# Optimization experiments

Measured on AMD Instinct MI355X. Metric: run time of the kernel, lower is better.

Reference implementation:

```python
import jax, jax.numpy as jnp
import numpy as np

N_NODES = 100000
N_EDGES = 3200000
IN_DIM, HID_DIM, OUT_DIM = 768, 50, 2


def gcn_conv(x, W, b, row, col, deg_isqrt, n_nodes):
    # PyG GCNConv: h = x @ W, then symmetric-normalized scatter-add (self-loops
    # already included in row/col), then + bias.
    h = x @ W                                    # [N, out]
    norm = deg_isqrt[row] * deg_isqrt[col]       # [E+N]
    msgs = h[row] * norm[:, None]                # gather + scale
    out = jax.ops.segment_sum(msgs, col, num_segments=n_nodes)
    return out + b


def _augment(edge_index, n_nodes):
    # add self-loops and compute D^{-1/2} with self-loops
    loops = jnp.arange(n_nodes, dtype=edge_index.dtype)
    row = jnp.concatenate([edge_index[0], loops])
    col = jnp.concatenate([edge_index[1], loops])
    deg = jax.ops.segment_sum(jnp.ones_like(col, dtype=jnp.float32), col,
                              num_segments=n_nodes)
    deg_isqrt = jnp.where(deg > 0, jax.lax.rsqrt(deg), 0.0)
    return row, col, deg_isqrt


def setup_inputs() -> dict:
    key = jax.random.key(0)
    k1, k2, k3, k4 = jax.random.split(key, 4)
    x = jax.random.normal(k1, (N_NODES, IN_DIM), dtype=jnp.float32)
    edge_index = jax.random.randint(k2, (2, N_EDGES), 0, N_NODES, dtype=jnp.int64)
    W1 = jax.random.normal(k3, (IN_DIM, HID_DIM), dtype=jnp.float32) / np.sqrt(IN_DIM)
    b1 = jnp.zeros((HID_DIM,), dtype=jnp.float32)
    W2 = jax.random.normal(k4, (HID_DIM, OUT_DIM), dtype=jnp.float32) / np.sqrt(HID_DIM)
    b2 = jnp.zeros((OUT_DIM,), dtype=jnp.float32)
    return {"x": x, "edge_index": edge_index, "W1": W1, "b1": b1, "W2": W2, "b2": b2}


def reference(x, edge_index, W1, b1, W2, b2):
    n = x.shape[0]
    row, col, deg_isqrt = _augment(edge_index, n)
    h = gcn_conv(x, W1, b1, row, col, deg_isqrt, n)   # GCNConv(768 -> 50)
    h = jax.nn.relu(h)                                 # ReLU
    h = gcn_conv(h, W2, b2, row, col, deg_isqrt, n)   # GCNConv(50 -> 2)
    return jax.nn.sigmoid(h)                           # Sigmoid output layer
```

## Files before the change

### kernel.cpp

```cpp
#include <hip/hip_runtime.h>


#define N_NODES 100000
#define N_EDGES 3200000
#define IN_DIM  768
#define HID     50
#define HIDP    52
#define SCAN_BLK 1024
#define NSCAN_BLKS 98
#define NPAD (NSCAN_BLKS * SCAN_BLK)

using s8v = __attribute__((ext_vector_type(8))) short;
using f4v = __attribute__((ext_vector_type(4))) float;

__device__ __forceinline__ short f2bf(float f) {
  union { float f; unsigned u; } v; v.f = f;
  unsigned r = (v.u + 0x7fffu + ((v.u >> 16) & 1u)) >> 16;
  return (short)r;
}
__device__ __forceinline__ float bf2f(unsigned short u) {
  union { unsigned u; float f; } v; v.u = ((unsigned)u) << 16;
  return v.f;
}


__global__ void k_init(int* __restrict__ cnt) {
  int g = blockIdx.x * 256 + threadIdx.x;
  if (g < NPAD) cnt[g] = 0;
}

__global__ void k_count(const int* __restrict__ edges, int* __restrict__ cnt) {
  int e = blockIdx.x * 256 + threadIdx.x;
  if (e < N_EDGES) atomicAdd(&cnt[edges[N_EDGES + e]], 1);
}

__global__ void k_scanA(const int* __restrict__ cnt, int* __restrict__ offs,
                        int* __restrict__ bsum) {
  __shared__ int s[SCAN_BLK];
  int t = threadIdx.x;
  int g = blockIdx.x * SCAN_BLK + t;
  int v = (g < N_NODES) ? cnt[g] : 0;
  s[t] = v;
  __syncthreads();
  for (int off = 1; off < SCAN_BLK; off <<= 1) {
    int add = (t >= off) ? s[t - off] : 0;
    __syncthreads();
    s[t] += add;
    __syncthreads();
  }
  offs[g] = s[t] - v;
  if (t == SCAN_BLK - 1) bsum[blockIdx.x] = s[t];
}

__global__ void k_scanB(int* __restrict__ bsum) {
  if (threadIdx.x == 0 && blockIdx.x == 0) {
    int acc = 0;
    for (int i = 0; i < NSCAN_BLKS; ++i) { int v = bsum[i]; bsum[i] = acc; acc += v; }
  }
}

__global__ void k_scanC(int* __restrict__ cnt, int* __restrict__ offs,
                        const int* __restrict__ bsum, float* __restrict__ dis) {
  int g = blockIdx.x * 256 + threadIdx.x;
  if (g < NPAD) {
    offs[g] += bsum[g >> 10];
    if (g < N_NODES) {
      dis[g] = rsqrtf((float)cnt[g] + 1.0f);
      cnt[g] = 0;
    }
  }
}

__global__ void k_fill(const int* __restrict__ edges, int* __restrict__ cnt,
                       const int* __restrict__ offs, int* __restrict__ eidx) {
  int e = blockIdx.x * 256 + threadIdx.x;
  if (e < N_EDGES) {
    int r = edges[e];
    int c = edges[N_EDGES + e];
    int p = atomicAdd(&cnt[c], 1);
    eidx[offs[c] + p] = r;
  }
}


__global__ __launch_bounds__(256) void k_gemm1(const float* __restrict__ x,
                                               const float* __restrict__ W1,
                                               unsigned short* __restrict__ h1) {
  __shared__ short BT[64][72];
  int t = threadIdx.x;
  int wave = t >> 6, lane = t & 63;
  int col = lane & 15, quad = lane >> 4;
  int rb = blockIdx.x * 64 + wave * 16;
  int arow = rb + col;
  if (arow > N_NODES - 1) arow = N_NODES - 1;
  const float* xrow = x + (size_t)arow * IN_DIM + quad * 8;

  f4v acc[4] = {f4v{0.f,0.f,0.f,0.f}, f4v{0.f,0.f,0.f,0.f},
                f4v{0.f,0.f,0.f,0.f}, f4v{0.f,0.f,0.f,0.f}};

  for (int chunk = 0; chunk < IN_DIM / 64; ++chunk) {
    int k0 = chunk * 64;
    __syncthreads();
    for (int e = t; e < 64 * 64; e += 256) {
      int k = e >> 6, n = e & 63;
      float v = (n < HID) ? W1[(k0 + k) * HID + n] : 0.f;
      BT[n][k] = f2bf(v);
    }
    __syncthreads();
    for (int kk = 0; kk < 64; kk += 32) {
      float4 va = *(const float4*)(xrow + k0 + kk);
      float4 vb = *(const float4*)(xrow + k0 + kk + 4);
      s8v a;
      a[0] = f2bf(va.x); a[1] = f2bf(va.y); a[2] = f2bf(va.z); a[3] = f2bf(va.w);
      a[4] = f2bf(vb.x); a[5] = f2bf(vb.y); a[6] = f2bf(vb.z); a[7] = f2bf(vb.w);
      s8v b0 = *(const s8v*)&BT[ 0 + col][kk + quad * 8];
      s8v b1 = *(const s8v*)&BT[16 + col][kk + quad * 8];
      s8v b2 = *(const s8v*)&BT[32 + col][kk + quad * 8];
      s8v b3 = *(const s8v*)&BT[48 + col][kk + quad * 8];
      acc[0] = __builtin_amdgcn_mfma_f32_16x16x32_bf16(a, b0, acc[0], 0, 0, 0);
      acc[1] = __builtin_amdgcn_mfma_f32_16x16x32_bf16(a, b1, acc[1], 0, 0, 0);
      acc[2] = __builtin_amdgcn_mfma_f32_16x16x32_bf16(a, b2, acc[2], 0, 0, 0);
      acc[3] = __builtin_amdgcn_mfma_f32_16x16x32_bf16(a, b3, acc[3], 0, 0, 0);
    }
  }
  for (int nt = 0; nt < 4; ++nt) {
    int c = nt * 16 + col;
    if (c < HIDP) {
      for (int r = 0; r < 4; ++r) {
        int node = rb + quad * 4 + r;
        if (node < N_NODES)
          h1[(size_t)node * HIDP + c] = (unsigned short)f2bf(acc[nt][r]);
      }
    }
  }
}


__global__ __launch_bounds__(256) void k_agg1(
    const unsigned short* __restrict__ h1, const int* __restrict__ eidx,
    const int* __restrict__ offs, const float* __restrict__ dis,
    const float* __restrict__ b1, const float* __restrict__ W2,
    float* __restrict__ h2) {
  __shared__ float W2s[2][HIDP];
  __shared__ float b1s[HIDP];
  int t = threadIdx.x;
  if (t < HIDP) {
    b1s[t] = (t < HID) ? b1[t] : 0.f;
    W2s[0][t] = (t < HID) ? W2[t * 2 + 0] : 0.f;
    W2s[1][t] = (t < HID) ? W2[t * 2 + 1] : 0.f;
  }
  __syncthreads();
  int g = t >> 4, L = t & 15;
  int n = blockIdx.x * 16 + g;
  if (n >= N_NODES) return;
  int start = offs[n];
  int end = (n == N_NODES - 1) ? N_EDGES : offs[n + 1];
  int base = L * 4;
  bool act = base < HIDP;
  float a0 = 0.f, a1 = 0.f, a2 = 0.f, a3 = 0.f;
  for (int i = start; i < end; ++i) {
    int idx = eidx[i];
    float d = dis[idx];
    if (act) {
      ushort4 u = *(const ushort4*)(h1 + (size_t)idx * HIDP + base);
      a0 += bf2f(u.x) * d; a1 += bf2f(u.y) * d;
      a2 += bf2f(u.z) * d; a3 += bf2f(u.w) * d;
    }
  }
  float p0 = 0.f, p1 = 0.f;
  if (act) {
    float dn = dis[n];
    ushort4 u = *(const ushort4*)(h1 + (size_t)n * HIDP + base);
    a0 = a0 * dn + bf2f(u.x) * dn * dn + b1s[base + 0];
    a1 = a1 * dn + bf2f(u.y) * dn * dn + b1s[base + 1];
    a2 = a2 * dn + bf2f(u.z) * dn * dn + b1s[base + 2];
    a3 = a3 * dn + bf2f(u.w) * dn * dn + b1s[base + 3];
    a0 = fmaxf(a0, 0.f); a1 = fmaxf(a1, 0.f);
    a2 = fmaxf(a2, 0.f); a3 = fmaxf(a3, 0.f);
    p0 = a0 * W2s[0][base] + a1 * W2s[0][base + 1] +
         a2 * W2s[0][base + 2] + a3 * W2s[0][base + 3];
    p1 = a0 * W2s[1][base] + a1 * W2s[1][base + 1] +
         a2 * W2s[1][base + 2] + a3 * W2s[1][base + 3];
  }
  for (int m = 8; m; m >>= 1) {
    p0 += __shfl_xor(p0, m, 16);
    p1 += __shfl_xor(p1, m, 16);
  }
  if (L == 0) {
    h2[(size_t)n * 2 + 0] = p0;
    h2[(size_t)n * 2 + 1] = p1;
  }
}


__global__ __launch_bounds__(256) void k_agg2(
    const float* __restrict__ h2, const int* __restrict__ eidx,
    const int* __restrict__ offs, const float* __restrict__ dis,
    const float* __restrict__ b2, float* __restrict__ out) {
  int t = threadIdx.x;
  int g = t >> 4, L = t & 15;
  int n = blockIdx.x * 16 + g;
  if (n >= N_NODES) return;
  int start = offs[n];
  int end = (n == N_NODES - 1) ? N_EDGES : offs[n + 1];
  float a0 = 0.f, a1 = 0.f;
  for (int i = start + L; i < end; i += 16) {
    int idx = eidx[i];
    float d = dis[idx];
    float2 v = *(const float2*)(h2 + (size_t)idx * 2);
    a0 += v.x * d; a1 += v.y * d;
  }
  for (int m = 8; m; m >>= 1) {
    a0 += __shfl_xor(a0, m, 16);
    a1 += __shfl_xor(a1, m, 16);
  }
  if (L == 0) {
    float dn = dis[n];
    float2 v = *(const float2*)(h2 + (size_t)n * 2);
    float r0 = a0 * dn + v.x * dn * dn + b2[0];
    float r1 = a1 * dn + v.y * dn * dn + b2[1];
    out[(size_t)n * 2 + 0] = 1.f / (1.f + __expf(-r0));
    out[(size_t)n * 2 + 1] = 1.f / (1.f + __expf(-r1));
  }
}


static inline size_t aln(size_t v) { return (v + 255) & ~(size_t)255; }

extern "C" void kernel_launch(void* const* d_in, const int* in_sizes, int n_in,
                              void* d_out, int out_size, void* d_ws, size_t ws_size,
                              hipStream_t stream) {
  const float* x     = (const float*)d_in[0];
  const int*   edges = (const int*)d_in[1];
  const float* W1    = (const float*)d_in[2];
  const float* b1    = (const float*)d_in[3];
  const float* W2    = (const float*)d_in[4];
  const float* b2    = (const float*)d_in[5];
  float* out = (float*)d_out;

  char* p = (char*)d_ws;
  int* cnt  = (int*)p;            p += aln((size_t)NPAD * 4);
  int* offs = (int*)p;            p += aln((size_t)NPAD * 4);
  int* bsum = (int*)p;            p += aln((size_t)NSCAN_BLKS * 4);
  float* dis = (float*)p;         p += aln((size_t)N_NODES * 4);
  int* eidx = (int*)p;            p += aln((size_t)N_EDGES * 4);
  unsigned short* h1 = (unsigned short*)p; p += aln((size_t)N_NODES * HIDP * 2);
  float* h2 = (float*)p;          p += aln((size_t)N_NODES * 2 * 4);

  int gN   = (NPAD + 255) / 256;
  int gE   = (N_EDGES + 255) / 256;
  int gMM  = (N_NODES + 63) / 64;
  int gAgg = (N_NODES + 15) / 16;

  k_init <<<gN, 256, 0, stream>>>(cnt);
  k_count<<<gE, 256, 0, stream>>>(edges, cnt);
  k_scanA<<<NSCAN_BLKS, SCAN_BLK, 0, stream>>>(cnt, offs, bsum);
  k_scanB<<<1, 64, 0, stream>>>(bsum);
  k_scanC<<<gN, 256, 0, stream>>>(cnt, offs, bsum, dis);
  k_fill <<<gE, 256, 0, stream>>>(edges, cnt, offs, eidx);
  k_gemm1<<<gMM, 256, 0, stream>>>(x, W1, h1);
  k_agg1 <<<gAgg, 256, 0, stream>>>(h1, eidx, offs, dis, b1, W2, h2);
  k_agg2 <<<gAgg, 256, 0, stream>>>(h2, eidx, offs, dis, b2, out);
}
```

Before: 938.9 us.

## Prescale features by source degree, prepack W1 fragments, widen aggregation to waves

h1 is now stored pre-multiplied by deg^-1/2 of the source node in the GEMM epilogue, so the aggregation loops no longer gather dis[idx] per edge. The same is done for the second-layer features. W1 is converted once into bf16 MFMA fragment order by a new prep kernel, which removes the per-block LDS transpose and its barriers from the GEMM. Each aggregation now uses one wave per node: agg1 splits edges four ways with a software-prefetched gather, and agg2 uses 64 lanes. The block-sum scan is parallelised and the counter init kernel becomes a memset. Per-node wave mapping may waste lanes on low-degree nodes, and the extra bf16 rounding after scaling slightly changes numerics.

Measured after the change: 839.2 us. 1.12x faster.

```diff
diff --git a/kernel.cpp b/kernel.cpp
--- a/kernel.cpp
+++ b/kernel.cpp
@@ -9,6 +9,7 @@
 #define SCAN_BLK 1024
 #define NSCAN_BLKS 98
 #define NPAD (NSCAN_BLKS * SCAN_BLK)
+#define NKSTEP (IN_DIM / 32)
 
 using s8v = __attribute__((ext_vector_type(8))) short;
 using f4v = __attribute__((ext_vector_type(4))) float;
@@ -23,11 +24,6 @@
   return v.f;
 }
 
-
-__global__ void k_init(int* __restrict__ cnt) {
-  int g = blockIdx.x * 256 + threadIdx.x;
-  if (g < NPAD) cnt[g] = 0;
-}
 
 __global__ void k_count(const int* __restrict__ edges, int* __restrict__ cnt) {
   int e = blockIdx.x * 256 + threadIdx.x;
@@ -53,10 +49,18 @@
 }
 
 __global__ void k_scanB(int* __restrict__ bsum) {
-  if (threadIdx.x == 0 && blockIdx.x == 0) {
-    int acc = 0;
-    for (int i = 0; i < NSCAN_BLKS; ++i) { int v = bsum[i]; bsum[i] = acc; acc += v; }
-  }
+  __shared__ int s[128];
+  int t = threadIdx.x;
+  int v = (t < NSCAN_BLKS) ? bsum[t] : 0;
+  s[t] = v;
+  __syncthreads();
+  for (int off = 1; off < 128; off <<= 1) {
+    int add = (t >= off) ? s[t - off] : 0;
+    __syncthreads();
+    s[t] += add;
+    __syncthreads();
+  }
+  if (t < NSCAN_BLKS) bsum[t] = s[t] - v;
 }
 
 __global__ void k_scanC(int* __restrict__ cnt, int* __restrict__ offs,
@@ -83,10 +87,25 @@
 }
 
 
+__global__ void k_wprep(const float* __restrict__ W1, short* __restrict__ Bfrag) {
+  int g = blockIdx.x * 256 + threadIdx.x;
+  int s = g >> 8, r = g & 255;
+  int nt = r >> 6, l = r & 63;
+  int col = l & 15, quad = l >> 4;
+  int n = nt * 16 + col;
+  int kb = s * 32 + quad * 8;
+  s8v o;
+#pragma unroll
+  for (int j = 0; j < 8; ++j)
+    o[j] = (n < HID) ? f2bf(W1[(size_t)(kb + j) * HID + n]) : (short)0;
+  *(s8v*)(Bfrag + (size_t)g * 8) = o;
+}
+
+
 __global__ __launch_bounds__(256) void k_gemm1(const float* __restrict__ x,
-                                               const float* __restrict__ W1,
+                                               const short* __restrict__ Bfrag,
+                                               const float* __restrict__ dis,
                                                unsigned short* __restrict__ h1) {
-  __shared__ short BT[64][72];
   int t = threadIdx.x;
   int wave = t >> 6, lane = t & 63;
   int col = lane & 15, quad = lane >> 4;
@@ -94,42 +113,42 @@
   int arow = rb + col;
   if (arow > N_NODES - 1) arow = N_NODES - 1;
   const float* xrow = x + (size_t)arow * IN_DIM + quad * 8;
+  const short* bbase = Bfrag + (size_t)lane * 8;
 
   f4v acc[4] = {f4v{0.f,0.f,0.f,0.f}, f4v{0.f,0.f,0.f,0.f},
                 f4v{0.f,0.f,0.f,0.f}, f4v{0.f,0.f,0.f,0.f}};
 
-  for (int chunk = 0; chunk < IN_DIM / 64; ++chunk) {
-    int k0 = chunk * 64;
-    __syncthreads();
-    for (int e = t; e < 64 * 64; e += 256) {
-      int k = e >> 6, n = e & 63;
-      float v = (n < HID) ? W1[(k0 + k) * HID + n] : 0.f;
-      BT[n][k] = f2bf(v);
-    }
-    __syncthreads();
-    for (int kk = 0; kk < 64; kk += 32) {
-      float4 va = *(const float4*)(xrow + k0 + kk);
-      float4 vb = *(const float4*)(xrow + k0 + kk + 4);
-      s8v a;
-      a[0] = f2bf(va.x); a[1] = f2bf(va.y); a[2] = f2bf(va.z); a[3] = f2bf(va.w);
-      a[4] = f2bf(vb.x); a[5] = f2bf(vb.y); a[6] = f2bf(vb.z); a[7] = f2bf(vb.w);
-      s8v b0 = *(const s8v*)&BT[ 0 + col][kk + quad * 8];
-      s8v b1 = *(const s8v*)&BT[16 + col][kk + quad * 8];
-      s8v b2 = *(const s8v*)&BT[32 + col][kk + quad * 8];
-      s8v b3 = *(const s8v*)&BT[48 + col][kk + quad * 8];
-      acc[0] = __builtin_amdgcn_mfma_f32_16x16x32_bf16(a, b0, acc[0], 0, 0, 0);
-      acc[1] = __builtin_amdgcn_mfma_f32_16x16x32_bf16(a, b1, acc[1], 0, 0, 0);
-      acc[2] = __builtin_amdgcn_mfma_f32_16x16x32_bf16(a, b2, acc[2], 0, 0, 0);
-      acc[3] = __builtin_amdgcn_mfma_f32_16x16x32_bf16(a, b3, acc[3], 0, 0, 0);
-    }
-  }
+#pragma unroll
+  for (int s = 0; s < NKSTEP; ++s) {
+    float4 va = *(const float4*)(xrow + s * 32);
+    float4 vb = *(const float4*)(xrow + s * 32 + 4);
+    s8v b0 = *(const s8v*)(bbase + (size_t)(s * 4 + 0) * 512);
+    s8v b1 = *(const s8v*)(bbase + (size_t)(s * 4 + 1) * 512);
+    s8v b2 = *(const s8v*)(bbase + (size_t)(s * 4 + 2) * 512);
+    s8v b3 = *(const s8v*)(bbase + (size_t)(s * 4 + 3) * 512);
+    s8v a;
+    a[0] = f2bf(va.x); a[1] = f2bf(va.y); a[2] = f2bf(va.z); a[3] = f2bf(va.w);
+    a[4] = f2bf(vb.x); a[5] = f2bf(vb.y); a[6] = f2bf(vb.z); a[7] = f2bf(vb.w);
+    acc[0] = __builtin_amdgcn_mfma_f32_16x16x32_bf16(a, b0, acc[0], 0, 0, 0);
+    acc[1] = __builtin_amdgcn_mfma_f32_16x16x32_bf16(a, b1, acc[1], 0, 0, 0);
+    acc[2] = __builtin_amdgcn_mfma_f32_16x16x32_bf16(a, b2, acc[2], 0, 0, 0);
+    acc[3] = __builtin_amdgcn_mfma_f32_16x16x32_bf16(a, b3, acc[3], 0, 0, 0);
+  }
+
+  int node0 = rb + quad * 4;
+  float dd[4];
+#pragma unroll
+  for (int r = 0; r < 4; ++r)
+    dd[r] = (node0 + r < N_NODES) ? dis[node0 + r] : 0.f;
+#pragma unroll
   for (int nt = 0; nt < 4; ++nt) {
     int c = nt * 16 + col;
     if (c < HIDP) {
+#pragma unroll
       for (int r = 0; r < 4; ++r) {
-        int node = rb + quad * 4 + r;
+        int node = node0 + r;
         if (node < N_NODES)
-          h1[(size_t)node * HIDP + c] = (unsigned short)f2bf(acc[nt][r]);
+          h1[(size_t)node * HIDP + c] = (unsigned short)f2bf(acc[nt][r] * dd[r]);
       }
     }
   }
@@ -140,85 +159,97 @@
     const unsigned short* __restrict__ h1, const int* __restrict__ eidx,
     const int* __restrict__ offs, const float* __restrict__ dis,
     const float* __restrict__ b1, const float* __restrict__ W2,
-    float* __restrict__ h2) {
-  __shared__ float W2s[2][HIDP];
-  __shared__ float b1s[HIDP];
-  int t = threadIdx.x;
-  if (t < HIDP) {
+    float* __restrict__ h2s) {
+  __shared__ float W2s[2][64];
+  __shared__ float b1s[64];
+  int t = threadIdx.x;
+  if (t < 64) {
     b1s[t] = (t < HID) ? b1[t] : 0.f;
     W2s[0][t] = (t < HID) ? W2[t * 2 + 0] : 0.f;
     W2s[1][t] = (t < HID) ? W2[t * 2 + 1] : 0.f;
   }
   __syncthreads();
-  int g = t >> 4, L = t & 15;
-  int n = blockIdx.x * 16 + g;
+  int wave = t >> 6, lane = t & 63;
+  int n = blockIdx.x * 4 + wave;
+  if (n >= N_NODES) return;
+  int way = lane >> 4, L = lane & 15;
+  int base = L * 4;
+  bool actC = base < HIDP;
+  int baseS = actC ? base : 0;
+  int start = offs[n];
+  int end = (n == N_NODES - 1) ? N_EDGES : offs[n + 1];
+
+  float a0 = 0.f, a1 = 0.f, a2 = 0.f, a3 = 0.f;
+  int i  = start + way;
+  int idx  = (i  < end) ? eidx[i]  : n;
+  ushort4 u = *(const ushort4*)(h1 + (size_t)idx * HIDP + baseS);
+  int i2 = i + 4;
+  int idx2 = (i2 < end) ? eidx[i2] : n;
+  while (i < end) {
+    ushort4 u2 = *(const ushort4*)(h1 + (size_t)idx2 * HIDP + baseS);
+    int i3 = i2 + 4;
+    int idx3 = (i3 < end) ? eidx[i3] : n;
+    a0 += bf2f(u.x); a1 += bf2f(u.y); a2 += bf2f(u.z); a3 += bf2f(u.w);
+    u = u2; idx2 = idx3; i = i2; i2 = i3;
+  }
+
+  a0 += __shfl_xor(a0, 16); a0 += __shfl_xor(a0, 32);
+  a1 += __shfl_xor(a1, 16); a1 += __shfl_xor(a1, 32);
+  a2 += __shfl_xor(a2, 16); a2 += __shfl_xor(a2, 32);
+  a3 += __shfl_xor(a3, 16); a3 += __shfl_xor(a3, 32);
+
+  float p0 = 0.f, p1 = 0.f;
+  if (actC && way == 0) {
+    float dn = dis[n];
+    ushort4 us = *(const ushort4*)(h1 + (size_t)n * HIDP + base);
+    float s0 = (a0 + bf2f(us.x)) * dn + b1s[base + 0];
+    float s1 = (a1 + bf2f(us.y)) * dn + b1s[base + 1];
+    float s2 = (a2 + bf2f(us.z)) * dn + b1s[base + 2];
+    float s3 = (a3 + bf2f(us.w)) * dn + b1s[base + 3];
+    s0 = fmaxf(s0, 0.f); s1 = fmaxf(s1, 0.f);
+    s2 = fmaxf(s2, 0.f); s3 = fmaxf(s3, 0.f);
+    p0 = s0 * W2s[0][base] + s1 * W2s[0][base + 1] +
+         s2 * W2s[0][base + 2] + s3 * W2s[0][base + 3];
+    p1 = s0 * W2s[1][base] + s1 * W2s[1][base + 1] +
+         s2 * W2s[1][base + 2] + s3 * W2s[1][base + 3];
+  }
+  for (int m = 8; m; m >>= 1) {
+    p0 += __shfl_xor(p0, m, 16);
+    p1 += __shfl_xor(p1, m, 16);
+  }
+  if (lane == 0) {
+    float dn = dis[n];
+    h2s[(size_t)n * 2 + 0] = p0 * dn;
+    h2s[(size_t)n * 2 + 1] = p1 * dn;
+  }
+}
+
+
+__global__ __launch_bounds__(256) void k_agg2(
+    const float* __restrict__ h2s, const int* __restrict__ eidx,
+    const int* __restrict__ offs, const float* __restrict__ dis,
+    const float* __restrict__ b2, float* __restrict__ out) {
+  int t = threadIdx.x;
+  int wave = t >> 6, lane = t & 63;
+  int n = blockIdx.x * 4 + wave;
   if (n >= N_NODES) return;
   int start = offs[n];
   int end = (n == N_NODES - 1) ? N_EDGES : offs[n + 1];
-  int base = L * 4;
-  bool act = base < HIDP;
-  float a0 = 0.f, a1 = 0.f, a2 = 0.f, a3 = 0.f;
-  for (int i = start; i < end; ++i) {
+  float s0 = 0.f, s1 = 0.f;
+  for (int i = start + lane; i < end; i += 64) {
     int idx = eidx[i];
-    float d = dis[idx];
-    if (act) {
-      ushort4 u = *(const ushort4*)(h1 + (size_t)idx * HIDP + base);
-      a0 += bf2f(u.x) * d; a1 += bf2f(u.y) * d;
-      a2 += bf2f(u.z) * d; a3 += bf2f(u.w) * d;
-    }
-  }
-  float p0 = 0.f, p1 = 0.f;
-  if (act) {
+    float2 v = *(const float2*)(h2s + (size_t)idx * 2);
+    s0 += v.x; s1 += v.y;
+  }
+  for (int m = 32; m; m >>= 1) {
+    s0 += __shfl_xor(s0, m);
+    s1 += __shfl_xor(s1, m);
+  }
+  if (lane == 0) {
     float dn = dis[n];
-    ushort4 u = *(const ushort4*)(h1 + (size_t)n * HIDP + base);
-    a0 = a0 * dn + bf2f(u.x) * dn * dn + b1s[base + 0];
-    a1 = a1 * dn + bf2f(u.y) * dn * dn + b1s[base + 1];
-    a2 = a2 * dn + bf2f(u.z) * dn * dn + b1s[base + 2];
-    a3 = a3 * dn + bf2f(u.w) * dn * dn + b1s[base + 3];
-    a0 = fmaxf(a0, 0.f); a1 = fmaxf(a1, 0.f);
-    a2 = fmaxf(a2, 0.f); a3 = fmaxf(a3, 0.f);
-    p0 = a0 * W2s[0][base] + a1 * W2s[0][base + 1] +
-         a2 * W2s[0][base + 2] + a3 * W2s[0][base + 3];
-    p1 = a0 * W2s[1][base] + a1 * W2s[1][base + 1] +
-         a2 * W2s[1][base + 2] + a3 * W2s[1][base + 3];
-  }
-  for (int m = 8; m; m >>= 1) {
-    p0 += __shfl_xor(p0, m, 16);
-    p1 += __shfl_xor(p1, m, 16);
-  }
-  if (L == 0) {
-    h2[(size_t)n * 2 + 0] = p0;
-    h2[(size_t)n * 2 + 1] = p1;
-  }
-}
-
-
-__global__ __launch_bounds__(256) void k_agg2(
-    const float* __restrict__ h2, const int* __restrict__ eidx,
-    const int* __restrict__ offs, const float* __restrict__ dis,
-    const float* __restrict__ b2, float* __restrict__ out) {
-  int t = threadIdx.x;
-  int g = t >> 4, L = t & 15;
-  int n = blockIdx.x * 16 + g;
-  if (n >= N_NODES) return;
-  int start = offs[n];
-  int end = (n == N_NODES - 1) ? N_EDGES : offs[n + 1];
-  float a0 = 0.f, a1 = 0.f;
-  for (int i = start + L; i < end; i += 16) {
-    int idx = eidx[i];
-    float d = dis[idx];
-    float2 v = *(const float2*)(h2 + (size_t)idx * 2);
-    a0 += v.x * d; a1 += v.y * d;
-  }
-  for (int m = 8; m; m >>= 1) {
-    a0 += __shfl_xor(a0, m, 16);
-    a1 += __shfl_xor(a1, m, 16);
-  }
-  if (L == 0) {
-    float dn = dis[n];
-    float2 v = *(const float2*)(h2 + (size_t)n * 2);
-    float r0 = a0 * dn + v.x * dn * dn + b2[0];
-    float r1 = a1 * dn + v.y * dn * dn + b2[1];
+    float2 v = *(const float2*)(h2s + (size_t)n * 2);
+    float r0 = (s0 + v.x) * dn + b2[0];
+    float r1 = (s1 + v.y) * dn + b2[1];
     out[(size_t)n * 2 + 0] = 1.f / (1.f + __expf(-r0));
     out[(size_t)n * 2 + 1] = 1.f / (1.f + __expf(-r1));
   }
@@ -244,21 +275,23 @@
   int* bsum = (int*)p;            p += aln((size_t)NSCAN_BLKS * 4);
   float* dis = (float*)p;         p += aln((size_t)N_NODES * 4);
   int* eidx = (int*)p;            p += aln((size_t)N_EDGES * 4);
+  short* Bfrag = (short*)p;       p += aln((size_t)NKSTEP * 4 * 64 * 8 * 2);
   unsigned short* h1 = (unsigned short*)p; p += aln((size_t)N_NODES * HIDP * 2);
-  float* h2 = (float*)p;          p += aln((size_t)N_NODES * 2 * 4);
+  float* h2s = (float*)p;         p += aln((size_t)N_NODES * 2 * 4);
 
   int gN   = (NPAD + 255) / 256;
   int gE   = (N_EDGES + 255) / 256;
   int gMM  = (N_NODES + 63) / 64;
-  int gAgg = (N_NODES + 15) / 16;
-
-  k_init <<<gN, 256, 0, stream>>>(cnt);
+  int gW   = (N_NODES + 3) / 4;
+
+  hipMemsetAsync(cnt, 0, (size_t)NPAD * 4, stream);
   k_count<<<gE, 256, 0, stream>>>(edges, cnt);
   k_scanA<<<NSCAN_BLKS, SCAN_BLK, 0, stream>>>(cnt, offs, bsum);
-  k_scanB<<<1, 64, 0, stream>>>(bsum);
+  k_scanB<<<1, 128, 0, stream>>>(bsum);
   k_scanC<<<gN, 256, 0, stream>>>(cnt, offs, bsum, dis);
   k_fill <<<gE, 256, 0, stream>>>(edges, cnt, offs, eidx);
-  k_gemm1<<<gMM, 256, 0, stream>>>(x, W1, h1);
-  k_agg1 <<<gAgg, 256, 0, stream>>>(h1, eidx, offs, dis, b1, W2, h2);
-  k_agg2 <<<gAgg, 256, 0, stream>>>(h2, eidx, offs, dis, b2, out);
-}
+  k_wprep<<<NKSTEP, 256, 0, stream>>>(W1, Bfrag);
+  k_gemm1<<<gMM, 256, 0, stream>>>(x, Bfrag, dis, h1);
+  k_agg1 <<<gW, 256, 0, stream>>>(h1, eidx, offs, dis, b1, W2, h2s);
+  k_agg2 <<<gW, 256, 0, stream>>>(h2s, eidx, offs, dis, b2, out);
+}
```
